# Kernel optimization log

Hardware: AMD Instinct MI355X
Metric: run time of the kernel (lower is better)

## Reference

```python
import jax, jax.numpy as jnp
import numpy as np

B, S, D_IN, D_OUT = 8, 2048, 768, 768
SCALE = float(D_IN) ** 0.5  # module divides by embed_size**0.5 where embed_size = input_dim


def setup_inputs() -> dict:
    key = jax.random.key(0)
    ks = jax.random.split(key, 8)
    std = 1.0 / np.sqrt(D_IN)
    return {
        "x": jax.random.normal(ks[0], (B, S, D_IN), dtype=jnp.float32),
        "mask": jax.random.randint(ks[1], (B, S), 0, 2, dtype=jnp.int32),
        "Wq": jax.random.normal(ks[2], (D_OUT, D_IN), dtype=jnp.float32) * std,
        "bq": jax.random.normal(ks[3], (D_OUT,), dtype=jnp.float32) * std,
        "Wk": jax.random.normal(ks[4], (D_OUT, D_IN), dtype=jnp.float32) * std,
        "bk": jax.random.normal(ks[5], (D_OUT,), dtype=jnp.float32) * std,
        "Wv": jax.random.normal(ks[6], (D_OUT, D_IN), dtype=jnp.float32) * std,
        "bv": jax.random.normal(ks[7], (D_OUT,), dtype=jnp.float32) * std,
    }


def reference(x, mask, Wq, bq, Wk, bk, Wv, bv):
    # QKV projections: nn.Linear computes x @ W.T + b
    Q = jnp.einsum("bsd,od->bso", x, Wq) + bq  # [B,S,D_OUT]
    K = jnp.einsum("bsd,od->bso", x, Wk) + bk
    V = jnp.einsum("bsd,od->bso", x, Wv) + bv
    scores = jnp.einsum("bqo,bko->bqk", Q, K) / SCALE  # [B,S,S]
    # key-position mask broadcast over query dim
    scores = jnp.where(mask[:, None, :] == 0, -jnp.inf, scores)
    weights = jax.nn.softmax(scores, axis=-1)
    out = jnp.einsum("bqk,bko->bqo", weights, V)  # [B,S,D_OUT]
    return out.mean(axis=1, keepdims=True)  # [B,1,D_OUT]
```

## Files before the change

kernel.cpp:

```cpp
#include <hip/hip_runtime.h>
#include <hip/hip_bf16.h>


#define S 2048
#define DIM 768
#define BATCH 8

typedef __hip_bfloat16 bf16;
typedef __attribute__((ext_vector_type(8))) short bf16x8;
typedef __attribute__((ext_vector_type(4))) short short4v;
typedef __attribute__((ext_vector_type(4))) float f32x4;

__device__ __forceinline__ f32x4 mfma16(bf16x8 a, bf16x8 b, f32x4 c) {
  return __builtin_amdgcn_mfma_f32_16x16x32_bf16(a, b, c, 0, 0, 0);
}

__device__ __forceinline__ void load_lds16(const short* g, short* l) {
  __builtin_amdgcn_global_load_lds(
      (const __attribute__((address_space(1))) unsigned int*)g,
      (__attribute__((address_space(3))) unsigned int*)l, 16, 0, 0);
}

__device__ __forceinline__ float b2f(short u) {
  union { float f; unsigned u; } v;
  v.u = ((unsigned)(unsigned short)u) << 16;
  return v.f;
}

__device__ __forceinline__ short f2b(float f) {
  bf16 h = __float2bfloat16(f);
  return *(short*)&h;
}

#define INV_SCALE 0.03608439182435161f

__global__ __launch_bounds__(256) void detect_dtype(const unsigned short* __restrict__ x,
                                                    int* __restrict__ flag) {
  int bad = 0;
  for (int i = threadIdx.x; i < 2048; i += 256) {
    int e = (x[i] >> 7) & 0xFF;
    if (e < 0x60 || e >= 0x9F) bad = 1;
  }
  if (bad) atomicOr(flag, 1);
}

__global__ __launch_bounds__(256) void prep_kernel(const void* __restrict__ Wq_raw,
                                                   const void* __restrict__ Wk_raw,
                                                   const void* __restrict__ bq_raw,
                                                   bf16* __restrict__ T0,
                                                   bf16* __restrict__ T1,
                                                   float* __restrict__ bvec,
                                                   const int* __restrict__ flag) {
  const int f = *flag;
  const int bx = blockIdx.x;
  if (bx < 288) {
    __shared__ unsigned short tile[64][66];
    const int p = bx / 144, r = bx % 144;
    const void* src = p ? Wk_raw : Wq_raw;
    unsigned short* dst = (unsigned short*)(p ? T1 : T0);
    const int obase = (r / 12) * 64, ibase = (r % 12) * 64;
    const int col = threadIdx.x & 63, rq = threadIdx.x >> 6;
#pragma unroll
    for (int rr = 0; rr < 64; rr += 4) {
      const long idx = (long)(obase + rr + rq) * DIM + ibase + col;
      const float v = f ? ((const float*)src)[idx] : b2f(((const short*)src)[idx]);
      tile[rr + rq][col] = (unsigned short)f2b(v);
    }
    __syncthreads();
#pragma unroll
    for (int rr = 0; rr < 64; rr += 4)
      dst[(long)(ibase + rr + rq) * DIM + obase + col] = tile[col][rr + rq];
  } else {
    const int o0 = (bx - 288) * 128;
    const int t = threadIdx.x;
    float s0 = 0.f, s1 = 0.f, s2 = 0.f;
    if (f) {
      const float* W = (const float*)Wk_raw;
      const float* bq = (const float*)bq_raw;
      for (int o = o0; o < o0 + 128; ++o) {
        const float bo = bq[o];
        const float* row = W + (long)o * DIM;
        s0 += row[t] * bo;
        s1 += row[t + 256] * bo;
        s2 += row[t + 512] * bo;
      }
    } else {
      const short* W = (const short*)Wk_raw;
      const short* bq = (const short*)bq_raw;
      for (int o = o0; o < o0 + 128; ++o) {
        const float bo = b2f(bq[o]);
        const short* row = W + (long)o * DIM;
        s0 += b2f(row[t]) * bo;
        s1 += b2f(row[t + 256]) * bo;
        s2 += b2f(row[t + 512]) * bo;
      }
    }
    atomicAdd(&bvec[t], s0);
    atomicAdd(&bvec[t + 256], s1);
    atomicAdd(&bvec[t + 512], s2);
  }
}

#define TILE_DECLS                                                          \
  __shared__ short As[4096], Bs[4096];                                      \
  const int tid = threadIdx.x;                                              \
  const int wave = tid >> 6, lane = tid & 63;                               \
  const int lr = lane & 15, quad = lane >> 4;                               \
  const int wm = (wave >> 1) * 64, wn = (wave & 1) * 64;                    \
  const int c0row = tid >> 2, colw = (tid & 3) * 8;

#define TILE_KLOOP(Abase, Bbase)                                            \
  const short* Ag0 = (Abase) + (long)(mblk + c0row) * DIM + colw;           \
  const short* Ag1 = (Abase) + (long)(mblk + 64 + c0row) * DIM + colw;      \
  const short* Bg0 = (Bbase) + (long)(nblk + c0row) * DIM + colw;           \
  const short* Bg1 = (Bbase) + (long)(nblk + 64 + c0row) * DIM + colw;      \
  short* Al0 = As + tid * 8;                                                \
  short* Al1 = As + 2048 + tid * 8;                                         \
  short* Bl0 = Bs + tid * 8;                                                \
  short* Bl1 = Bs + 2048 + tid * 8;                                         \
  f32x4 acc[4][4] = {};                                                     \
  for (int k0 = 0; k0 < DIM; k0 += 32) {                                    \
    load_lds16(Ag0 + k0, Al0);                                              \
    load_lds16(Ag1 + k0, Al1);                                              \
    load_lds16(Bg0 + k0, Bl0);                                              \
    load_lds16(Bg1 + k0, Bl1);                                              \
    asm volatile("s_waitcnt vmcnt(0)" ::: "memory");                        \
    __syncthreads();                                                        \
    bf16x8 af[4], bfr[4];                                                   \
    _Pragma("unroll") for (int it = 0; it < 4; ++it)                        \
        af[it] = *(const bf16x8*)(As + (wm + it * 16 + lr) * 32 + quad * 8);\
    _Pragma("unroll") for (int jt = 0; jt < 4; ++jt)                        \
        bfr[jt] = *(const bf16x8*)(Bs + (wn + jt * 16 + lr) * 32 + quad * 8);\
    _Pragma("unroll") for (int it = 0; it < 4; ++it)                        \
        _Pragma("unroll") for (int jt = 0; jt < 4; ++jt)                    \
            acc[it][jt] = mfma16(af[it], bfr[jt], acc[it][jt]);             \
    __syncthreads();                                                        \
  }

__global__ __launch_bounds__(256) void mt_convert(const bf16* __restrict__ WkT,
                                                  const bf16* __restrict__ WqT,
                                                  bf16* __restrict__ Mt,
                                                  const void* __restrict__ x_raw,
                                                  const int* __restrict__ mask,
                                                  const float* __restrict__ bvec,
                                                  bf16* __restrict__ xb,
                                                  float* __restrict__ betas,
                                                  const int* __restrict__ flag) {
  const int bx = blockIdx.x;
  if (bx < 36) {
    const int mblk = (bx / 6) * 128, nblk = (bx % 6) * 128;
    TILE_DECLS
    TILE_KLOOP((const short*)WkT, (const short*)WqT)
#pragma unroll
    for (int it = 0; it < 4; ++it)
#pragma unroll
      for (int jt = 0; jt < 4; ++jt)
#pragma unroll
        for (int r = 0; r < 4; ++r)
          Mt[(long)(mblk + wm + it * 16 + quad * 4 + r) * DIM +
             nblk + wn + jt * 16 + lr] = __float2bfloat16(acc[it][jt][r]);
  } else {
    const int wave = threadIdx.x >> 6, lane = threadIdx.x & 63;
    const int n = (bx - 36) * 4 + wave;
    const int f = *flag;
    short* xo = (short*)xb + (long)n * DIM;
    float s = 0.f;
    if (f) {
      const float4* x4 = (const float4*)((const float*)x_raw + (long)n * DIM);
      const float4* bv4 = (const float4*)bvec;
#pragma unroll
      for (int it = 0; it < 3; ++it) {
        const int idx = it * 64 + lane;
        const float4 v = x4[idx];
        const float4 bb = bv4[idx];
        short4v sv = {f2b(v.x), f2b(v.y), f2b(v.z), f2b(v.w)};
        *(short4v*)(xo + idx * 4) = sv;
        s += v.x * bb.x + v.y * bb.y + v.z * bb.z + v.w * bb.w;
      }
    } else {
      const short4v* x4 = (const short4v*)((const short*)x_raw + (long)n * DIM);
      const float4* bv4 = (const float4*)bvec;
#pragma unroll
      for (int it = 0; it < 3; ++it) {
        const int idx = it * 64 + lane;
        const short4v v = x4[idx];
        const float4 bb = bv4[idx];
        *(short4v*)(xo + idx * 4) = v;
        s += b2f(v.x) * bb.x + b2f(v.y) * bb.y + b2f(v.z) * bb.z + b2f(v.w) * bb.w;
      }
    }
#pragma unroll
    for (int off = 1; off < 64; off <<= 1) s += __shfl_xor(s, off, 64);
    if (lane == 0) betas[n] = mask[n] ? s * INV_SCALE : -1e30f;
  }
}


#define BARX() asm volatile("s_barrier" ::: "memory")
#define LGKM0() asm volatile("s_waitcnt lgkmcnt(0)" ::: "memory")
#define VMC4() asm volatile("s_waitcnt vmcnt(4)" ::: "memory")
#define VMC0() asm volatile("s_waitcnt vmcnt(0)" ::: "memory")

__device__ __forceinline__ void core256(const short* A, const short* B,
                                        short* sh, f32x4 (&acc)[8][4],
                                        const int wm, const int wn,
                                        const int lr, const int quad,
                                        const int tid) {
  const int sw7 = lr & 7;
  const int cof0 = (quad ^ sw7) * 8;
  const int cof1 = ((quad + 4) ^ sw7) * 8;
  const int rS = tid >> 3;
  const int cS8 = ((tid & 7) ^ (rS & 7)) * 8;
  const short* aP0 = A + (long)rS * DIM + cS8;
  const short* aP1 = aP0 + 128 * DIM;
  const short* bP0 = B + (long)rS * DIM + cS8;
  const short* bP1 = bP0 + 128 * DIM;
  short* l0 = sh + tid * 8;
  short* l1 = sh + 4096 + tid * 8;
  bf16x8 af0[4][2], af1[4][2], bf0[2][2], bf1[2][2];

#define STG(BASE, GP, K0)                              \
  do {                                                 \
    load_lds16((GP) + (K0), l0 + (BASE));              \
    load_lds16((GP) + 64 * DIM + (K0), l1 + (BASE));   \
  } while (0)
#define READ_AF0(AB)                                                \
  _Pragma("unroll") for (int f_ = 0; f_ < 4; ++f_) {                \
    const int ro_ = (AB) + (wm + f_ * 16 + lr) * 64;                \
    af0[f_][0] = *(const bf16x8*)(sh + ro_ + cof0);                 \
    af0[f_][1] = *(const bf16x8*)(sh + ro_ + cof1);                 \
  }
#define READ_AF1(AB)                                                \
  _Pragma("unroll") for (int f_ = 0; f_ < 4; ++f_) {                \
    const int ro_ = (AB) + (wm + 64 + f_ * 16 + lr) * 64;           \
    af1[f_][0] = *(const bf16x8*)(sh + ro_ + cof0);                 \
    af1[f_][1] = *(const bf16x8*)(sh + ro_ + cof1);                 \
  }
#define READ_BF0(BB)                                                \
  _Pragma("unroll") for (int f_ = 0; f_ < 2; ++f_) {                \
    const int ro_ = (BB) + (wn + f_ * 16 + lr) * 64;                \
    bf0[f_][0] = *(const bf16x8*)(sh + ro_ + cof0);                 \
    bf0[f_][1] = *(const bf16x8*)(sh + ro_ + cof1);                 \
  }
#define READ_BF1(BB)                                                \
  _Pragma("unroll") for (int f_ = 0; f_ < 2; ++f_) {                \
    const int ro_ = (BB) + (wn + 32 + f_ * 16 + lr) * 64;           \
    bf1[f_][0] = *(const bf16x8*)(sh + ro_ + cof0);                 \
    bf1[f_][1] = *(const bf16x8*)(sh + ro_ + cof1);                 \
  }
#define MMA8(AF, BF, FIO, FJO)                                            \
  _Pragma("unroll") for (int i_ = 0; i_ < 4; ++i_)                        \
  _Pragma("unroll") for (int j_ = 0; j_ < 2; ++j_) {                      \
    acc[i_ + (FIO)][j_ + (FJO)] =                                         \
        mfma16(AF[i_][0], BF[j_][0], acc[i_ + (FIO)][j_ + (FJO)]);        \
    acc[i_ + (FIO)][j_ + (FJO)] =                                         \
        mfma16(AF[i_][1], BF[j_][1], acc[i_ + (FIO)][j_ + (FJO)]);        \
  }

  STG(16384, bP0, 0); STG(24576, bP1, 0);
  STG(0, aP0, 0);     STG(8192, aP1, 0);
  STG(49152, bP0, 64); STG(57344, bP1, 64);
  VMC4();
  BARX();

#pragma unroll 1
  for (int t = 0; t < 5; ++t) {
    const int kA1 = (2 * t + 1) * 64;
    const int kB2 = kA1 + 64;
    const int kB3 = kB2 + 64;
    READ_AF0(0) READ_BF0(16384)
    STG(32768, aP0, kA1);
    BARX(); LGKM0(); __builtin_amdgcn_s_setprio(1);
    MMA8(af0, bf0, 0, 0) __builtin_amdgcn_s_setprio(0); BARX();
    READ_BF1(16384)
    STG(40960, aP1, kA1);
    BARX(); LGKM0(); __builtin_amdgcn_s_setprio(1);
    MMA8(af0, bf1, 0, 2) __builtin_amdgcn_s_setprio(0); BARX();
    READ_AF1(0)
    STG(16384, bP0, kB2);
    BARX(); LGKM0(); __builtin_amdgcn_s_setprio(1);
    MMA8(af1, bf0, 4, 0) __builtin_amdgcn_s_setprio(0); BARX();
    STG(24576, bP1, kB2);
    VMC4();
    BARX(); __builtin_amdgcn_s_setprio(1);
    MMA8(af1, bf1, 4, 2) __builtin_amdgcn_s_setprio(0); BARX();
    READ_AF0(32768) READ_BF0(49152)
    STG(0, aP0, kB2);
    BARX(); LGKM0(); __builtin_amdgcn_s_setprio(1);
    MMA8(af0, bf0, 0, 0) __builtin_amdgcn_s_setprio(0); BARX();
    READ_BF1(49152)
    STG(8192, aP1, kB2);
    BARX(); LGKM0(); __builtin_amdgcn_s_setprio(1);
    MMA8(af0, bf1, 0, 2) __builtin_amdgcn_s_setprio(0); BARX();
    READ_AF1(32768)
    STG(49152, bP0, kB3);
    BARX(); LGKM0(); __builtin_amdgcn_s_setprio(1);
    MMA8(af1, bf0, 4, 0) __builtin_amdgcn_s_setprio(0); BARX();
    STG(57344, bP1, kB3);
    VMC4();
    BARX(); __builtin_amdgcn_s_setprio(1);
    MMA8(af1, bf1, 4, 2) __builtin_amdgcn_s_setprio(0); BARX();
  }

  READ_AF0(0) READ_BF0(16384)
  STG(32768, aP0, 704);
  BARX(); LGKM0(); __builtin_amdgcn_s_setprio(1);
  MMA8(af0, bf0, 0, 0) __builtin_amdgcn_s_setprio(0); BARX();
  READ_BF1(16384)
  STG(40960, aP1, 704);
  BARX(); LGKM0(); __builtin_amdgcn_s_setprio(1);
  MMA8(af0, bf1, 0, 2) __builtin_amdgcn_s_setprio(0); BARX();
  READ_AF1(0)
  BARX(); LGKM0(); __builtin_amdgcn_s_setprio(1);
  MMA8(af1, bf0, 4, 0) __builtin_amdgcn_s_setprio(0); BARX();
  VMC0();
  BARX(); __builtin_amdgcn_s_setprio(1);
  MMA8(af1, bf1, 4, 2) __builtin_amdgcn_s_setprio(0); BARX();
  READ_AF0(32768) READ_BF0(49152)
  BARX(); LGKM0(); __builtin_amdgcn_s_setprio(1);
  MMA8(af0, bf0, 0, 0) __builtin_amdgcn_s_setprio(0); BARX();
  READ_BF1(49152)
  BARX(); LGKM0(); __builtin_amdgcn_s_setprio(1);
  MMA8(af0, bf1, 0, 2) __builtin_amdgcn_s_setprio(0); BARX();
  READ_AF1(32768)
  BARX(); LGKM0(); __builtin_amdgcn_s_setprio(1);
  MMA8(af1, bf0, 4, 0) __builtin_amdgcn_s_setprio(0); BARX();
  __builtin_amdgcn_s_setprio(1);
  MMA8(af1, bf1, 4, 2) __builtin_amdgcn_s_setprio(0);

#undef STG
#undef READ_AF0
#undef READ_AF1
#undef READ_BF0
#undef READ_BF1
#undef MMA8
}

__global__ __launch_bounds__(512, 2) void gemm_nt_256(const bf16* __restrict__ A,
                                                      const bf16* __restrict__ B,
                                                      bf16* __restrict__ D) {
  __shared__ __align__(16) short sh[65536];
  const int tid = threadIdx.x;
  const int wave = tid >> 6, lane = tid & 63;
  const int lr = lane & 15, quad = lane >> 4;
  const int wm = (wave >> 2) * 128, wn = (wave & 3) * 64;
  const int mblk = blockIdx.x * 256, nblk = blockIdx.y * 256;
  f32x4 acc[8][4] = {};
  core256((const short*)A + (long)mblk * DIM, (const short*)B + (long)nblk * DIM,
          sh, acc, wm, wn, lr, quad, tid);
#pragma unroll
  for (int fi = 0; fi < 8; ++fi)
#pragma unroll
    for (int fj = 0; fj < 4; ++fj)
#pragma unroll
      for (int r = 0; r < 4; ++r)
        D[(long)(mblk + wm + fi * 16 + quad * 4 + r) * DIM +
          nblk + wn + fj * 16 + lr] = __float2bfloat16(acc[fi][fj][r]);
}

__global__ __launch_bounds__(512, 2) void gemm_score_256(const bf16* __restrict__ z,
                                                         const bf16* __restrict__ x,
                                                         const float* __restrict__ betas,
                                                         float* __restrict__ l_out,
                                                         bf16* __restrict__ E,
                                                         int b0) {
  __shared__ __align__(16) short sh[65536];
  const int nwg = (int)gridDim.x;
  const int cpx = nwg >> 3;
  const int bid = (blockIdx.x & 7) * cpx + (blockIdx.x >> 3);
  const int lb = bid >> 6, rb = bid & 63;
  const int mblk = (rb >> 3) * 256, nblk = (rb & 7) * 256;
  const int b = b0 + lb;
  const int tid = threadIdx.x;
  const int wave = tid >> 6, lane = tid & 63;
  const int lr = lane & 15, quad = lane >> 4;
  const int wm = (wave >> 2) * 128, wn = (wave & 3) * 64;
  f32x4 acc[8][4] = {};
  core256((const short*)z + (long)lb * S * DIM + (long)mblk * DIM,
          (const short*)x + (long)b * S * DIM + (long)nblk * DIM,
          sh, acc, wm, wn, lr, quad, tid);
  float bet[4];
#pragma unroll
  for (int fj = 0; fj < 4; ++fj)
    bet[fj] = betas[b * S + nblk + wn + fj * 16 + lr];
  bf16* Eb = E + (long)lb * S * S;
  float* lrow = l_out + b * S;
#pragma unroll
  for (int fi = 0; fi < 8; ++fi) {
#pragma unroll
    for (int r = 0; r < 4; ++r) {
      const int q = mblk + wm + fi * 16 + quad * 4 + r;
      float s = 0.f;
#pragma unroll
      for (int fj = 0; fj < 4; ++fj) {
        float e = __expf(fminf(acc[fi][fj][r] * INV_SCALE + bet[fj], 60.f));
        s += e;
        Eb[(long)q * S + nblk + wn + fj * 16 + lr] = __float2bfloat16(e);
      }
      s += __shfl_xor(s, 1, 64);
      s += __shfl_xor(s, 2, 64);
      s += __shfl_xor(s, 4, 64);
      s += __shfl_xor(s, 8, 64);
      if (lr == 0) atomicAdd(&lrow[q], s);
    }
  }
}

__global__ __launch_bounds__(256) void reduce_c(const bf16* __restrict__ E,
                                                const float* __restrict__ l,
                                                float* __restrict__ c, int b0) {
  const int lb = blockIdx.y, b = b0 + lb;
  const int q0 = blockIdx.x * 16;
  const int k8 = threadIdx.x * 8;
  const short* Eb = (const short*)E + (long)lb * S * S + k8;
  const float* lrow = l + b * S;
  float acc[8] = {};
#pragma unroll
  for (int q = q0; q < q0 + 16; ++q) {
    bf16x8 ev = *(const bf16x8*)(Eb + (long)q * S);
    const float lv = lrow[q];
    const float rq = lv > 0.f ? 1.0f / lv : 0.f;
#pragma unroll
    for (int j = 0; j < 8; ++j) acc[j] += b2f(ev[j]) * rq;
  }
#pragma unroll
  for (int j = 0; j < 8; ++j)
    atomicAdd(&c[b * S + k8 + j], acc[j] * (1.0f / 2048.0f));
}

__global__ __launch_bounds__(256) void y_kernel(const bf16* __restrict__ x,
                                                const float* __restrict__ c,
                                                float* __restrict__ y) {
  const int b = blockIdx.z;
  const int i = blockIdx.x * 256 + threadIdx.x;
  const int kstart = blockIdx.y * 128;
  const bf16* xb = x + (long)(b * S + kstart) * DIM + i;
  const float* cb = c + b * S + kstart;
  float acc = 0.f;
  for (int k = 0; k < 128; ++k)
    acc += cb[k] * __bfloat162float(xb[(long)k * DIM]);
  atomicAdd(&y[b * DIM + i], acc);
}

__global__ __launch_bounds__(256) void out_kernel(const float* __restrict__ y,
                                                  const void* __restrict__ Wv_raw,
                                                  const void* __restrict__ bv_raw,
                                                  void* __restrict__ out,
                                                  const int* __restrict__ flag) {
  const int wave = threadIdx.x >> 6, lane = threadIdx.x & 63;
  const int w = blockIdx.x * 4 + wave;
  const int b = w / DIM, o = w % DIM;
  const int f = *flag;
  const float4* y4 = (const float4*)(y + (long)b * DIM);
  float s = 0.f;
  if (f) {
    const float4* wr = (const float4*)((const float*)Wv_raw + (long)o * DIM);
#pragma unroll
    for (int it = 0; it < 3; ++it) {
      const int idx = it * 64 + lane;
      const float4 a = y4[idx], wv = wr[idx];
      s += a.x * wv.x + a.y * wv.y + a.z * wv.z + a.w * wv.w;
    }
  } else {
    const short4v* wr = (const short4v*)((const short*)Wv_raw + (long)o * DIM);
#pragma unroll
    for (int it = 0; it < 3; ++it) {
      const int idx = it * 64 + lane;
      const float4 a = y4[idx];
      const short4v wv = wr[idx];
      s += a.x * b2f(wv.x) + a.y * b2f(wv.y) + a.z * b2f(wv.z) + a.w * b2f(wv.w);
    }
  }
#pragma unroll
  for (int off = 1; off < 64; off <<= 1) s += __shfl_xor(s, off, 64);
  if (lane == 0) {
    const float bias = f ? ((const float*)bv_raw)[o] : b2f(((const short*)bv_raw)[o]);
    const float v = s + bias;
    if (f) ((float*)out)[b * DIM + o] = v;
    else ((bf16*)out)[b * DIM + o] = __float2bfloat16(v);
  }
}

extern "C" void kernel_launch(void* const* d_in, const int* in_sizes, int n_in,
                              void* d_out, int out_size, void* d_ws, size_t ws_size,
                              hipStream_t stream) {
  const void* x_raw = d_in[0];
  const int* mask = (const int*)d_in[1];
  const void* Wq_raw = d_in[2];
  const void* bq_raw = d_in[3];
  const void* Wk_raw = d_in[4];
  const void* Wv_raw = d_in[6];
  const void* bv_raw = d_in[7];

  char* ws = (char*)d_ws;
  bf16* xb = (bf16*)(ws);
  bf16* WqT = (bf16*)(ws + 25165824);
  bf16* WkT = (bf16*)(ws + 26345472);
  bf16* Mt = (bf16*)(ws + 27525120);
  float* betas = (float*)(ws + 28704768);
  float* bvec = (float*)(ws + 28770304);
  float* l = (float*)(ws + 28773376);
  float* c = (float*)(ws + 28838912);
  float* y = (float*)(ws + 28904448);
  int* flag = (int*)(ws + 28929024);
  bf16* z = (bf16*)(ws + 28929088);

  const size_t fixed = 28929088;
  const size_t zb = 3145728, eb = 8388608;
  int nb = 1;
  if (ws_size >= fixed + 8 * (zb + eb)) nb = 8;
  else if (ws_size >= fixed + 4 * (zb + eb)) nb = 4;
  else if (ws_size >= fixed + 2 * (zb + eb)) nb = 2;
  bf16* E = (bf16*)(ws + fixed + (size_t)nb * zb);
  const int rounds = BATCH / nb;

  (void)hipMemsetAsync(bvec, 0, 3072 + 65536 + 65536 + 24576 + 64, stream);

  detect_dtype<<<1, 256, 0, stream>>>((const unsigned short*)x_raw, flag);
  prep_kernel<<<294, 256, 0, stream>>>(Wq_raw, Wk_raw, bq_raw, WqT, WkT, bvec, flag);
  mt_convert<<<4132, 256, 0, stream>>>(WkT, WqT, Mt, x_raw, mask, bvec, xb,
                                       betas, flag);

  for (int r = 0; r < rounds; ++r) {
    const int b0 = r * nb;
    gemm_nt_256<<<dim3(nb * 8, 3), 512, 0, stream>>>(
        xb + (long)b0 * S * DIM, Mt, z);
    gemm_score_256<<<nb * 64, 512, 0, stream>>>(z, xb, betas, l, E, b0);
    reduce_c<<<dim3(128, nb), 256, 0, stream>>>(E, l, c, b0);
  }

  y_kernel<<<dim3(3, 16, 8), 256, 0, stream>>>(xb, c, y);
  out_kernel<<<1536, 256, 0, stream>>>(y, Wv_raw, bv_raw, d_out, flag);
}
```

Before: 316.6 us.

## Recompute score GEMM in a second pass instead of materializing exp-score matrix

The score kernel no longer stores the bf16 exp(score) matrix E. It only accumulates the row sums l. A new second pass recomputes the same z·x^T GEMM tile, weights each exp by the reciprocal row sum, and reduces over queries in registers, shuffles and LDS into the column vector c. This removes the large S×S E write and read and the separate reduce_c kernel. In exchange the GEMM compute and the exp work are done twice. The smaller workspace footprint may also let more batches run per round.

Measured after the change: 270.1 us. -14.7%, faster.

```diff
diff --git a/kernel.cpp b/kernel.cpp
--- a/kernel.cpp
+++ b/kernel.cpp
@@ -358,12 +358,11 @@
           nblk + wn + fj * 16 + lr] = __float2bfloat16(acc[fi][fj][r]);
 }
 
-__global__ __launch_bounds__(512, 2) void gemm_score_256(const bf16* __restrict__ z,
-                                                         const bf16* __restrict__ x,
-                                                         const float* __restrict__ betas,
-                                                         float* __restrict__ l_out,
-                                                         bf16* __restrict__ E,
-                                                         int b0) {
+__global__ __launch_bounds__(512, 2) void gemm_pass1(const bf16* __restrict__ z,
+                                                     const bf16* __restrict__ x,
+                                                     const float* __restrict__ betas,
+                                                     float* __restrict__ l_out,
+                                                     int b0) {
   __shared__ __align__(16) short sh[65536];
   const int nwg = (int)gridDim.x;
   const int cpx = nwg >> 3;
@@ -383,7 +382,6 @@
 #pragma unroll
   for (int fj = 0; fj < 4; ++fj)
     bet[fj] = betas[b * S + nblk + wn + fj * 16 + lr];
-  bf16* Eb = E + (long)lb * S * S;
   float* lrow = l_out + b * S;
 #pragma unroll
   for (int fi = 0; fi < 8; ++fi) {
@@ -392,11 +390,8 @@
       const int q = mblk + wm + fi * 16 + quad * 4 + r;
       float s = 0.f;
 #pragma unroll
-      for (int fj = 0; fj < 4; ++fj) {
-        float e = __expf(fminf(acc[fi][fj][r] * INV_SCALE + bet[fj], 60.f));
-        s += e;
-        Eb[(long)q * S + nblk + wn + fj * 16 + lr] = __float2bfloat16(e);
-      }
+      for (int fj = 0; fj < 4; ++fj)
+        s += __expf(fminf(acc[fi][fj][r] * INV_SCALE + bet[fj], 60.f));
       s += __shfl_xor(s, 1, 64);
       s += __shfl_xor(s, 2, 64);
       s += __shfl_xor(s, 4, 64);
@@ -406,26 +401,66 @@
   }
 }
 
-__global__ __launch_bounds__(256) void reduce_c(const bf16* __restrict__ E,
-                                                const float* __restrict__ l,
-                                                float* __restrict__ c, int b0) {
-  const int lb = blockIdx.y, b = b0 + lb;
-  const int q0 = blockIdx.x * 16;
-  const int k8 = threadIdx.x * 8;
-  const short* Eb = (const short*)E + (long)lb * S * S + k8;
-  const float* lrow = l + b * S;
-  float acc[8] = {};
-#pragma unroll
-  for (int q = q0; q < q0 + 16; ++q) {
-    bf16x8 ev = *(const bf16x8*)(Eb + (long)q * S);
-    const float lv = lrow[q];
-    const float rq = lv > 0.f ? 1.0f / lv : 0.f;
-#pragma unroll
-    for (int j = 0; j < 8; ++j) acc[j] += b2f(ev[j]) * rq;
-  }
-#pragma unroll
-  for (int j = 0; j < 8; ++j)
-    atomicAdd(&c[b * S + k8 + j], acc[j] * (1.0f / 2048.0f));
+__global__ __launch_bounds__(512, 2) void gemm_pass2(const bf16* __restrict__ z,
+                                                     const bf16* __restrict__ x,
+                                                     const float* __restrict__ betas,
+                                                     const float* __restrict__ l,
+                                                     float* __restrict__ c,
+                                                     int b0) {
+  __shared__ __align__(16) short sh[65536];
+  const int nwg = (int)gridDim.x;
+  const int cpx = nwg >> 3;
+  const int bid = (blockIdx.x & 7) * cpx + (blockIdx.x >> 3);
+  const int lb = bid >> 6, rb = bid & 63;
+  const int mblk = (rb >> 3) * 256, nblk = (rb & 7) * 256;
+  const int b = b0 + lb;
+  const int tid = threadIdx.x;
+  const int wave = tid >> 6, lane = tid & 63;
+  const int lr = lane & 15, quad = lane >> 4;
+  const int wm = (wave >> 2) * 128, wn = (wave & 3) * 64;
+  f32x4 acc[8][4] = {};
+  core256((const short*)z + (long)lb * S * DIM + (long)mblk * DIM,
+          (const short*)x + (long)b * S * DIM + (long)nblk * DIM,
+          sh, acc, wm, wn, lr, quad, tid);
+  float* lds_rq = (float*)sh;
+  float* cred = (float*)sh + 256;
+  if (tid < 256) {
+    const float lv = l[b * S + mblk + tid];
+    lds_rq[tid] = lv > 0.f ? 1.0f / lv : 0.f;
+  }
+  float bet[4];
+#pragma unroll
+  for (int fj = 0; fj < 4; ++fj)
+    bet[fj] = betas[b * S + nblk + wn + fj * 16 + lr];
+  __syncthreads();
+  float csum[4] = {};
+#pragma unroll
+  for (int fi = 0; fi < 8; ++fi) {
+#pragma unroll
+    for (int r = 0; r < 4; ++r) {
+      const float rqv = lds_rq[wm + fi * 16 + quad * 4 + r];
+#pragma unroll
+      for (int fj = 0; fj < 4; ++fj)
+        csum[fj] += __expf(fminf(acc[fi][fj][r] * INV_SCALE + bet[fj], 60.f)) * rqv;
+    }
+  }
+#pragma unroll
+  for (int fj = 0; fj < 4; ++fj) {
+    csum[fj] += __shfl_xor(csum[fj], 16, 64);
+    csum[fj] += __shfl_xor(csum[fj], 32, 64);
+  }
+  if (wave >= 4 && quad == 0) {
+#pragma unroll
+    for (int fj = 0; fj < 4; ++fj)
+      cred[((wave & 3) * 4 + fj) * 16 + lr] = csum[fj];
+  }
+  __syncthreads();
+  if (wave < 4 && quad == 0) {
+#pragma unroll
+    for (int fj = 0; fj < 4; ++fj)
+      atomicAdd(&c[b * S + nblk + wn + fj * 16 + lr],
+                (csum[fj] + cred[(wave * 4 + fj) * 16 + lr]) * (1.0f / 2048.0f));
+  }
 }
 
 __global__ __launch_bounds__(256) void y_kernel(const bf16* __restrict__ x,
@@ -506,12 +541,11 @@
   bf16* z = (bf16*)(ws + 28929088);
 
   const size_t fixed = 28929088;
-  const size_t zb = 3145728, eb = 8388608;
+  const size_t zb = 3145728;
   int nb = 1;
-  if (ws_size >= fixed + 8 * (zb + eb)) nb = 8;
-  else if (ws_size >= fixed + 4 * (zb + eb)) nb = 4;
-  else if (ws_size >= fixed + 2 * (zb + eb)) nb = 2;
-  bf16* E = (bf16*)(ws + fixed + (size_t)nb * zb);
+  if (ws_size >= fixed + 8 * zb) nb = 8;
+  else if (ws_size >= fixed + 4 * zb) nb = 4;
+  else if (ws_size >= fixed + 2 * zb) nb = 2;
   const int rounds = BATCH / nb;
 
   (void)hipMemsetAsync(bvec, 0, 3072 + 65536 + 65536 + 24576 + 64, stream);
@@ -525,8 +559,8 @@
     const int b0 = r * nb;
     gemm_nt_256<<<dim3(nb * 8, 3), 512, 0, stream>>>(
         xb + (long)b0 * S * DIM, Mt, z);
-    gemm_score_256<<<nb * 64, 512, 0, stream>>>(z, xb, betas, l, E, b0);
-    reduce_c<<<dim3(128, nb), 256, 0, stream>>>(E, l, c, b0);
+    gemm_pass1<<<nb * 64, 512, 0, stream>>>(z, xb, betas, l, b0);
+    gemm_pass2<<<nb * 64, 512, 0, stream>>>(z, xb, betas, l, c, b0);
   }
 
   y_kernel<<<dim3(3, 16, 8), 256, 0, stream>>>(xb, c, y);
```
